# Performance work log

Measured on AMD Instinct MI355X. Metric: run time of the kernel, lower is better.

## Reference

```python
import jax, jax.numpy as jnp
import numpy as np

BOX = 256
SIGMA = 1.5
KS = 9  # int(ceil(6*sigma)), made odd
N_POINTS = 20000
N_NEURONS = 32
N_LAYERS = 3
LATENT = 8
BATCH = 16


def _make_kernel2(ks, sigma):
    ax = np.arange(ks) - ks // 2
    yy, xx = np.meshgrid(ax, ax, indexing='ij')
    k = np.exp(-(xx ** 2 + yy ** 2) / (2.0 * sigma ** 2))
    return (k / k.sum()).astype(np.float32)


def setup_inputs() -> dict:
    key = jax.random.key(0)
    ks = jax.random.split(key, 16)
    def n(k, shape, scale=1.0):
        return scale * jax.random.normal(k, shape, dtype=jnp.float32)
    return {
        'z': n(ks[0], (BATCH, LATENT)),
        'r': n(ks[1], (BATCH, 3, 3)),
        'pos': 0.1 * (jax.random.uniform(ks[2], (N_POINTS, 3), dtype=jnp.float32) - 0.5),
        'amp': 0.1 * jnp.ones((1,), jnp.float32),
        'linamp1_W': n(ks[3], (N_NEURONS, 4), 0.3),
        'ampblock_W': n(ks[4], (N_LAYERS, N_NEURONS, N_NEURONS), 0.1),
        'ampblock_b': n(ks[5], (N_LAYERS, N_NEURONS), 0.05),
        'linamp2_W': n(ks[6], (1, N_NEURONS), 0.1),
        'linamp2_b': n(ks[7], (1,), 0.05),
        'lin0_W': n(ks[8], (N_NEURONS, 3 + LATENT - 1), 0.3),
        'deform_W': n(ks[9], (N_LAYERS, N_NEURONS, N_NEURONS), 0.1),
        'deform_b': n(ks[10], (N_LAYERS, N_NEURONS), 0.05),
        'lin1a_W': n(ks[11], (3, N_NEURONS), 0.2),
        'lin1b_W': n(ks[12], (3, 3), 0.2),
        'k2': jnp.asarray(_make_kernel2(KS, SIGMA)),
        'd': 1,
    }


def _res_mlp(x, Ws, bs):
    # residual blocks: x <- relu(x @ W^T + b) + x
    for i in range(Ws.shape[0]):
        x = jax.nn.relu(x @ Ws[i].T + bs[i]) + x
    return x


def _splat(proj, amps, k2):
    # Gaussian-kernel splat of points onto [B, BOX, BOX] images.
    # proj: [B,P,2] coords in ~[-0.5, 0.5]; amps: [B,P]; k2: [KS,KS]
    B, P, _ = proj.shape
    ks = k2.shape[0]
    half = ks // 2
    pix = (proj + 0.5) * (BOX - 1)
    cx = jnp.round(pix[..., 0]).astype(jnp.int32)
    cy = jnp.round(pix[..., 1]).astype(jnp.int32)
    offs = jnp.arange(ks, dtype=jnp.int32) - half
    oy, ox = jnp.meshgrid(offs, offs, indexing='ij')
    xx = cx[:, :, None] + ox.reshape(-1)[None, None, :]   # [B,P,ks*ks]
    yy = cy[:, :, None] + oy.reshape(-1)[None, None, :]
    w = amps[:, :, None] * k2.reshape(-1)[None, None, :]
    valid = (xx >= 0) & (xx < BOX) & (yy >= 0) & (yy < BOX)
    bidx = jnp.arange(B, dtype=jnp.int32)[:, None, None]
    flat = jnp.where(valid, (bidx * BOX + yy) * BOX + xx, 0)
    img = jnp.zeros((B * BOX * BOX,), proj.dtype).at[flat.reshape(-1)].add(
        jnp.where(valid, w, jnp.zeros_like(w)).reshape(-1))
    return img.reshape(B, BOX, BOX)


def _forward(z, r, pos, amp, linamp1_W, ampblock_W, ampblock_b, linamp2_W,
             linamp2_b, lin0_W, deform_W, deform_b, lin1a_W, lin1b_W, k2, d):
    B = z.shape[0]
    P = pos.shape[0]
    posi = jnp.broadcast_to(pos[None], (B, P, 3))
    # amplitude head (diff_conf=True): last latent channel per point
    conf_a = jnp.broadcast_to(z[:, -1:][:, None, :], (B, P, 1))
    a = jnp.concatenate([posi, conf_a], axis=-1) @ linamp1_W.T
    a = _res_mlp(a, ampblock_W, ampblock_b)
    amp_corr = jax.nn.sigmoid(a @ linamp2_W.T + linamp2_b)  # [B,P,1]
    # deformation head on remaining latent channels
    if d > 0:
        conf = jnp.broadcast_to(z[:, :-1][:, None, :], (B, P, z.shape[1] - 1))
        res = jnp.concatenate([posi, conf], axis=-1) @ lin0_W.T
        res = _res_mlp(res, deform_W, deform_b)
        res = jnp.tanh(res @ lin1a_W.T)
        res = res @ lin1b_W.T
        pos_def = posi + res
    else:
        res = jnp.zeros_like(posi)
        pos_def = posi
    # project rotated points to 2D
    proj_pos = jnp.einsum('bij,bpj->bpi', r, pos_def)[..., :2]
    amps = amp * amp_corr[..., 0]  # [B,P]
    proj_im = _splat(proj_pos, amps, k2)
    return proj_im, pos_def, res, amp_corr


def reference(z, r, pos, amp, linamp1_W, ampblock_W, ampblock_b, linamp2_W,
              linamp2_b, lin0_W, deform_W, deform_b, lin1a_W, lin1b_W, k2, d):
    return _forward(z, r, pos, amp, linamp1_W, ampblock_W, ampblock_b,
                    linamp2_W, linamp2_b, lin0_W, deform_W, deform_b,
                    lin1a_W, lin1b_W, k2, d)
```

## Files before the change

### kernel.cpp

```cpp
#include <hip/hip_runtime.h>

#define BOX   256
#define KS    9
#define HALF  4
#define NPTS  20000
#define NB    16
#define NN    32
#define NL    3
#define NLAT  8
#define CANW  (BOX + 2 * HALF)

typedef _Float16 half8   __attribute__((ext_vector_type(8)));
typedef float    floatx4 __attribute__((ext_vector_type(4)));

#define WH_ELEMS      8192
#define LINAMP2_OFF   16384
#define LIN1A_OFF     16512
#define G_OFF         16896
#define CANVAS_OFF    20480
#define CANVAS_F4     ((NB * CANW * CANW) / 4)

__device__ __forceinline__ int perm_inv(int k) {
    return ((k >> 2) & 1) * 16 + (k >> 3) * 4 + (k & 3);
}

__global__ __launch_bounds__(256) void prep_kernel(
    const float* __restrict__ linamp1_W, const float* __restrict__ ampblock_W,
    const float* __restrict__ lin0_W, const float* __restrict__ deform_W,
    const float* __restrict__ lin1a_W, const float* __restrict__ linamp2_W,
    const float* __restrict__ k2, char* __restrict__ ws)
{
    const int idx = blockIdx.x * 256 + threadIdx.x;

    if (idx < CANVAS_F4) {
        floatx4 zv = {0.f, 0.f, 0.f, 0.f};
        ((floatx4*)(ws + CANVAS_OFF))[idx] = zv;
    }

    if (idx < WH_ELEMS) {
        _Float16* wh = (_Float16*)ws;
        const int mat = idx >> 10, rem = idx & 1023;
        const int m = rem >> 5, k = rem & 31;
        float v = 0.0f;
        if (mat == 0)      { if (k < 4)  v = linamp1_W[m * 4 + k]; }
        else if (mat <= 3) { v = ampblock_W[(mat - 1) * 1024 + m * 32 + perm_inv(k)]; }
        else if (mat == 4) { if (k < 10) v = lin0_W[m * 10 + k]; }
        else               { v = deform_W[(mat - 5) * 1024 + m * 32 + perm_inv(k)]; }
        wh[idx] = (_Float16)v;
    } else if (idx < WH_ELEMS + 32) {
        const int k = idx - WH_ELEMS;
        ((float*)(ws + LINAMP2_OFF))[k] = linamp2_W[perm_inv(k)];
    } else if (idx < WH_ELEMS + 32 + 96) {
        const int t = idx - (WH_ELEMS + 32);
        const int i = t >> 5, k = t & 31;
        ((float*)(ws + LIN1A_OFF))[t] = lin1a_W[i * 32 + perm_inv(k)];
    } else if (idx < WH_ELEMS + 32 + 96 + 9) {
        const int i = idx - (WH_ELEMS + 32 + 96);
        float s = 0.0f;
        #pragma unroll
        for (int j = 0; j < KS; ++j) s += k2[i * KS + j];
        ((float*)(ws + G_OFF))[i] = s;
    }
}

__global__ __launch_bounds__(256) void point_kernel(
    const float* __restrict__ z, const float* __restrict__ r,
    const float* __restrict__ pos, const float* __restrict__ amp,
    const float* __restrict__ ampblock_b, const float* __restrict__ linamp2_b,
    const float* __restrict__ deform_b, const float* __restrict__ lin1b_W,
    const int* __restrict__ dflag, const char* __restrict__ ws,
    float* __restrict__ canvas, float* __restrict__ pos_def_out,
    float* __restrict__ res_out, float* __restrict__ amp_corr_out)
{
    const _Float16* wh       = (const _Float16*)ws;
    const float*    linamp2p = (const float*)(ws + LINAMP2_OFF);
    const float*    lin1ap   = (const float*)(ws + LIN1A_OFF);

    const int tid  = blockIdx.x * 256 + threadIdx.x;
    const int lane = threadIdx.x & 63;
    const int n    = lane & 15;
    const int quad = lane >> 4;
    const int w    = tid >> 6;
    const int base_bp = w * 16;
    const int b    = base_bp / NPTS;
    const int base_p = base_bp - b * NPTS;
    const int p    = base_p + n;
    const int bp   = base_bp + n;
    const int d    = *dflag;

    const float px = pos[3 * p + 0];
    const float py = pos[3 * p + 1];
    const float pz = pos[3 * p + 2];
    float zv[NLAT];
    #pragma unroll
    for (int i = 0; i < NLAT; ++i) zv[i] = z[b * NLAT + i];

    const floatx4 zero = {0.f, 0.f, 0.f, 0.f};
    const int aoff = quad * 8;

    float xB[8];
    {
        half8 bf;
        #pragma unroll
        for (int j = 0; j < 8; ++j) bf[j] = (_Float16)0.f;
        if (quad == 0) {
            bf[0] = (_Float16)px; bf[1] = (_Float16)py;
            bf[2] = (_Float16)pz; bf[3] = (_Float16)zv[NLAT - 1];
        }
        half8 a0 = *(const half8*)(wh + (n)      * 32 + aoff);
        half8 a1 = *(const half8*)(wh + (n + 16) * 32 + aoff);
        floatx4 c0 = __builtin_amdgcn_mfma_f32_16x16x32_f16(a0, bf, zero, 0, 0, 0);
        floatx4 c1 = __builtin_amdgcn_mfma_f32_16x16x32_f16(a1, bf, zero, 0, 0, 0);
        #pragma unroll
        for (int rr = 0; rr < 4; ++rr) { xB[rr] = c0[rr]; xB[4 + rr] = c1[rr]; }
    }
    #pragma unroll
    for (int l = 0; l < NL; ++l) {
        half8 hf;
        #pragma unroll
        for (int j = 0; j < 8; ++j) hf[j] = (_Float16)xB[j];
        const _Float16* M = wh + (1 + l) * 1024;
        half8 a0 = *(const half8*)(M + (n)      * 32 + aoff);
        half8 a1 = *(const half8*)(M + (n + 16) * 32 + aoff);
        floatx4 d0 = __builtin_amdgcn_mfma_f32_16x16x32_f16(a0, hf, zero, 0, 0, 0);
        floatx4 d1 = __builtin_amdgcn_mfma_f32_16x16x32_f16(a1, hf, zero, 0, 0, 0);
        floatx4 b0 = *(const floatx4*)(ampblock_b + l * 32 + quad * 4);
        floatx4 b1 = *(const floatx4*)(ampblock_b + l * 32 + 16 + quad * 4);
        #pragma unroll
        for (int rr = 0; rr < 4; ++rr) {
            xB[rr]     += fmaxf(d0[rr] + b0[rr], 0.f);
            xB[4 + rr] += fmaxf(d1[rr] + b1[rr], 0.f);
        }
    }
    float corr;
    {
        floatx4 wa = *(const floatx4*)(linamp2p + aoff);
        floatx4 wb = *(const floatx4*)(linamp2p + aoff + 4);
        float s = 0.f;
        #pragma unroll
        for (int rr = 0; rr < 4; ++rr) s += wa[rr] * xB[rr] + wb[rr] * xB[4 + rr];
        s += __shfl_xor(s, 16);
        s += __shfl_xor(s, 32);
        corr = 1.f / (1.f + __expf(-(s + linamp2_b[0])));
    }

    float r0 = 0.f, r1 = 0.f, r2 = 0.f;
    if (d > 0) {
        {
            half8 bf;
            #pragma unroll
            for (int j = 0; j < 8; ++j) bf[j] = (_Float16)0.f;
            if (quad == 0) {
                bf[0] = (_Float16)px;    bf[1] = (_Float16)py;
                bf[2] = (_Float16)pz;    bf[3] = (_Float16)zv[0];
                bf[4] = (_Float16)zv[1]; bf[5] = (_Float16)zv[2];
                bf[6] = (_Float16)zv[3]; bf[7] = (_Float16)zv[4];
            } else if (quad == 1) {
                bf[0] = (_Float16)zv[5]; bf[1] = (_Float16)zv[6];
            }
            const _Float16* M = wh + 4 * 1024;
            half8 a0 = *(const half8*)(M + (n)      * 32 + aoff);
            half8 a1 = *(const half8*)(M + (n + 16) * 32 + aoff);
            floatx4 c0 = __builtin_amdgcn_mfma_f32_16x16x32_f16(a0, bf, zero, 0, 0, 0);
            floatx4 c1 = __builtin_amdgcn_mfma_f32_16x16x32_f16(a1, bf, zero, 0, 0, 0);
            #pragma unroll
            for (int rr = 0; rr < 4; ++rr) { xB[rr] = c0[rr]; xB[4 + rr] = c1[rr]; }
        }
        #pragma unroll
        for (int l = 0; l < NL; ++l) {
            half8 hf;
            #pragma unroll
            for (int j = 0; j < 8; ++j) hf[j] = (_Float16)xB[j];
            const _Float16* M = wh + (5 + l) * 1024;
            half8 a0 = *(const half8*)(M + (n)      * 32 + aoff);
            half8 a1 = *(const half8*)(M + (n + 16) * 32 + aoff);
            floatx4 d0 = __builtin_amdgcn_mfma_f32_16x16x32_f16(a0, hf, zero, 0, 0, 0);
            floatx4 d1 = __builtin_amdgcn_mfma_f32_16x16x32_f16(a1, hf, zero, 0, 0, 0);
            floatx4 b0 = *(const floatx4*)(deform_b + l * 32 + quad * 4);
            floatx4 b1 = *(const floatx4*)(deform_b + l * 32 + 16 + quad * 4);
            #pragma unroll
            for (int rr = 0; rr < 4; ++rr) {
                xB[rr]     += fmaxf(d0[rr] + b0[rr], 0.f);
                xB[4 + rr] += fmaxf(d1[rr] + b1[rr], 0.f);
            }
        }
        float t3[3];
        #pragma unroll
        for (int i = 0; i < 3; ++i) {
            floatx4 wa = *(const floatx4*)(lin1ap + i * 32 + aoff);
            floatx4 wb = *(const floatx4*)(lin1ap + i * 32 + aoff + 4);
            float s = 0.f;
            #pragma unroll
            for (int rr = 0; rr < 4; ++rr) s += wa[rr] * xB[rr] + wb[rr] * xB[4 + rr];
            s += __shfl_xor(s, 16);
            s += __shfl_xor(s, 32);
            t3[i] = 1.f - 2.f / (__expf(2.f * s) + 1.f);
        }
        r0 = t3[0] * lin1b_W[0] + t3[1] * lin1b_W[1] + t3[2] * lin1b_W[2];
        r1 = t3[0] * lin1b_W[3] + t3[1] * lin1b_W[4] + t3[2] * lin1b_W[5];
        r2 = t3[0] * lin1b_W[6] + t3[1] * lin1b_W[7] + t3[2] * lin1b_W[8];
    }

    const float pdx = px + r0, pdy = py + r1, pdz = pz + r2;

    if (quad == 0) {
        pos_def_out[3 * bp + 0] = pdx;
        pos_def_out[3 * bp + 1] = pdy;
        pos_def_out[3 * bp + 2] = pdz;
    } else if (quad == 1) {
        res_out[3 * bp + 0] = r0;
        res_out[3 * bp + 1] = r1;
        res_out[3 * bp + 2] = r2;
    } else if (quad == 2) {
        amp_corr_out[bp] = corr;
    } else {
        const float* rb = r + b * 9;
        const float pjx = rb[0] * pdx + rb[1] * pdy + rb[2] * pdz;
        const float pjy = rb[3] * pdx + rb[4] * pdy + rb[5] * pdz;
        const int cx = (int)rintf((pjx + 0.5f) * (float)(BOX - 1));
        const int cy = (int)rintf((pjy + 0.5f) * (float)(BOX - 1));
        if (cx >= -HALF && cx <= BOX - 1 + HALF &&
            cy >= -HALF && cy <= BOX - 1 + HALF) {
            atomicAdd(canvas + ((size_t)b * CANW + (cy + HALF)) * CANW + (cx + HALF),
                      amp[0] * corr);
        }
    }
}

__global__ __launch_bounds__(256) void conv_kernel(
    const float* __restrict__ canvas, const float* __restrict__ gws,
    float* __restrict__ img)
{
    __shared__ float t_lds[24][256];
    const int x  = threadIdx.x;
    const int b  = blockIdx.x >> 4;
    const int y0 = (blockIdx.x & 15) * 16;

    float g[KS];
    #pragma unroll
    for (int i = 0; i < KS; ++i) g[i] = gws[i];

    const float* cb = canvas + (size_t)b * CANW * CANW;
    #pragma unroll 4
    for (int rr = 0; rr < 24; ++rr) {
        const float* row = cb + (size_t)(y0 + rr) * CANW;
        float s = 0.f;
        #pragma unroll
        for (int i = 0; i < KS; ++i) s = fmaf(g[i], row[x + (KS - 1) - i], s);
        t_lds[rr][x] = s;
    }
    __syncthreads();

    float* ib = img + ((size_t)b * BOX + y0) * BOX;
    #pragma unroll 4
    for (int yy = 0; yy < 16; ++yy) {
        float s = 0.f;
        #pragma unroll
        for (int i = 0; i < KS; ++i) s = fmaf(g[i], t_lds[yy + (KS - 1) - i][x], s);
        ib[yy * BOX + x] = s;
    }
}

extern "C" void kernel_launch(void* const* d_in, const int* in_sizes, int n_in,
                              void* d_out, int out_size, void* d_ws, size_t ws_size,
                              hipStream_t stream) {
    const float* z          = (const float*)d_in[0];
    const float* r          = (const float*)d_in[1];
    const float* pos        = (const float*)d_in[2];
    const float* amp        = (const float*)d_in[3];
    const float* linamp1_W  = (const float*)d_in[4];
    const float* ampblock_W = (const float*)d_in[5];
    const float* ampblock_b = (const float*)d_in[6];
    const float* linamp2_W  = (const float*)d_in[7];
    const float* linamp2_b  = (const float*)d_in[8];
    const float* lin0_W     = (const float*)d_in[9];
    const float* deform_W   = (const float*)d_in[10];
    const float* deform_b   = (const float*)d_in[11];
    const float* lin1a_W    = (const float*)d_in[12];
    const float* lin1b_W    = (const float*)d_in[13];
    const float* k2         = (const float*)d_in[14];
    const int*   dflag      = (const int*)d_in[15];

    float* out = (float*)d_out;
    float* img          = out;
    float* pos_def_out  = out + (size_t)NB * BOX * BOX;
    float* res_out      = pos_def_out + (size_t)NB * NPTS * 3;
    float* amp_corr_out = res_out + (size_t)NB * NPTS * 3;

    char*  ws     = (char*)d_ws;
    float* gws    = (float*)(ws + G_OFF);
    float* canvas = (float*)(ws + CANVAS_OFF);

    prep_kernel<<<(CANVAS_F4 + 255) / 256, 256, 0, stream>>>(
        linamp1_W, ampblock_W, lin0_W, deform_W, lin1a_W, linamp2_W, k2, ws);

    point_kernel<<<5000, 256, 0, stream>>>(
        z, r, pos, amp, ampblock_b, linamp2_b, deform_b, lin1b_W, dflag,
        ws, canvas, pos_def_out, res_out, amp_corr_out);

    conv_kernel<<<NB * 16, 256, 0, stream>>>(canvas, gws, img);
}
```

Before: 143.3 us.

## Fuse prep, point MLP and separable conv into one persistent mega-kernel

Replaces the three launches with one memset plus a single kernel. Each block stages the fp16 weight matrices and biases in LDS and runs four 16-point groups per wave so weight fragments are reused. The last 128 blocks to finish, found through an atomic ticket counter, spin until all blocks are done and then run the separable Gaussian conv from LDS-staged canvas rows. This removes the launch gaps and the global weight reads, but it adds spin-waiting, a larger per-block LDS footprint and more register pressure.

Result: slower. 201.6 us (+40.7%).

```diff
diff --git a/kernel.cpp b/kernel.cpp
--- a/kernel.cpp
+++ b/kernel.cpp
@@ -5,259 +5,296 @@
 #define HALF  4
 #define NPTS  20000
 #define NB    16
-#define NN    32
-#define NL    3
 #define NLAT  8
-#define CANW  (BOX + 2 * HALF)
+#define CANW  264
+#define NBLK  1250
+#define NCONV 128
+#define CANVAS_ELEMS (NB * CANW * CANW)
 
 typedef _Float16 half8   __attribute__((ext_vector_type(8)));
 typedef float    floatx4 __attribute__((ext_vector_type(4)));
 
-#define WH_ELEMS      8192
-#define LINAMP2_OFF   16384
-#define LIN1A_OFF     16512
-#define G_OFF         16896
-#define CANVAS_OFF    20480
-#define CANVAS_F4     ((NB * CANW * CANW) / 4)
+#define CANVAS_BYTE_OFF 16
+
+#define SM_BYTES 49920
 
 __device__ __forceinline__ int perm_inv(int k) {
     return ((k >> 2) & 1) * 16 + (k >> 3) * 4 + (k & 3);
 }
 
-__global__ __launch_bounds__(256) void prep_kernel(
+__global__ __launch_bounds__(256, 2) void mega_kernel(
+    const float* __restrict__ z, const float* __restrict__ r,
+    const float* __restrict__ pos, const float* __restrict__ amp,
     const float* __restrict__ linamp1_W, const float* __restrict__ ampblock_W,
-    const float* __restrict__ lin0_W, const float* __restrict__ deform_W,
-    const float* __restrict__ lin1a_W, const float* __restrict__ linamp2_W,
-    const float* __restrict__ k2, char* __restrict__ ws)
+    const float* __restrict__ ampblock_b, const float* __restrict__ linamp2_W,
+    const float* __restrict__ linamp2_b, const float* __restrict__ lin0_W,
+    const float* __restrict__ deform_W, const float* __restrict__ deform_b,
+    const float* __restrict__ lin1a_W, const float* __restrict__ lin1b_W,
+    const float* __restrict__ k2, const int* __restrict__ dflag,
+    int* __restrict__ counter, float* __restrict__ canvas,
+    float* __restrict__ img, float* __restrict__ pos_def_out,
+    float* __restrict__ res_out, float* __restrict__ amp_corr_out)
 {
-    const int idx = blockIdx.x * 256 + threadIdx.x;
-
-    if (idx < CANVAS_F4) {
-        floatx4 zv = {0.f, 0.f, 0.f, 0.f};
-        ((floatx4*)(ws + CANVAS_OFF))[idx] = zv;
-    }
-
-    if (idx < WH_ELEMS) {
-        _Float16* wh = (_Float16*)ws;
-        const int mat = idx >> 10, rem = idx & 1023;
-        const int m = rem >> 5, k = rem & 31;
-        float v = 0.0f;
+    __shared__ __align__(16) char smem[SM_BYTES];
+    __shared__ int s_tk;
+    _Float16* wh       = (_Float16*)smem;
+    float*    linamp2p = (float*)(smem + 16384);
+    float*    lin1ap   = (float*)(smem + 16512);
+    float*    ampb     = (float*)(smem + 16896);
+    float*    defb     = (float*)(smem + 17280);
+
+    for (int e = threadIdx.x; e < 8192; e += 256) {
+        const int mat = e >> 10, rem = e & 1023, m = rem >> 5, k = rem & 31;
+        float v = 0.f;
         if (mat == 0)      { if (k < 4)  v = linamp1_W[m * 4 + k]; }
         else if (mat <= 3) { v = ampblock_W[(mat - 1) * 1024 + m * 32 + perm_inv(k)]; }
         else if (mat == 4) { if (k < 10) v = lin0_W[m * 10 + k]; }
         else               { v = deform_W[(mat - 5) * 1024 + m * 32 + perm_inv(k)]; }
-        wh[idx] = (_Float16)v;
-    } else if (idx < WH_ELEMS + 32) {
-        const int k = idx - WH_ELEMS;
-        ((float*)(ws + LINAMP2_OFF))[k] = linamp2_W[perm_inv(k)];
-    } else if (idx < WH_ELEMS + 32 + 96) {
-        const int t = idx - (WH_ELEMS + 32);
-        const int i = t >> 5, k = t & 31;
-        ((float*)(ws + LIN1A_OFF))[t] = lin1a_W[i * 32 + perm_inv(k)];
-    } else if (idx < WH_ELEMS + 32 + 96 + 9) {
-        const int i = idx - (WH_ELEMS + 32 + 96);
-        float s = 0.0f;
-        #pragma unroll
-        for (int j = 0; j < KS; ++j) s += k2[i * KS + j];
-        ((float*)(ws + G_OFF))[i] = s;
-    }
-}
-
-__global__ __launch_bounds__(256) void point_kernel(
-    const float* __restrict__ z, const float* __restrict__ r,
-    const float* __restrict__ pos, const float* __restrict__ amp,
-    const float* __restrict__ ampblock_b, const float* __restrict__ linamp2_b,
-    const float* __restrict__ deform_b, const float* __restrict__ lin1b_W,
-    const int* __restrict__ dflag, const char* __restrict__ ws,
-    float* __restrict__ canvas, float* __restrict__ pos_def_out,
-    float* __restrict__ res_out, float* __restrict__ amp_corr_out)
-{
-    const _Float16* wh       = (const _Float16*)ws;
-    const float*    linamp2p = (const float*)(ws + LINAMP2_OFF);
-    const float*    lin1ap   = (const float*)(ws + LIN1A_OFF);
-
-    const int tid  = blockIdx.x * 256 + threadIdx.x;
+        wh[e] = (_Float16)v;
+    }
+    if (threadIdx.x < 32) linamp2p[threadIdx.x] = linamp2_W[perm_inv(threadIdx.x)];
+    if (threadIdx.x < 96) {
+        lin1ap[threadIdx.x] = lin1a_W[(threadIdx.x >> 5) * 32 + perm_inv(threadIdx.x & 31)];
+        ampb[threadIdx.x]   = ampblock_b[threadIdx.x];
+        defb[threadIdx.x]   = deform_b[threadIdx.x];
+    }
+    __syncthreads();
+
     const int lane = threadIdx.x & 63;
     const int n    = lane & 15;
     const int quad = lane >> 4;
-    const int w    = tid >> 6;
-    const int base_bp = w * 16;
-    const int b    = base_bp / NPTS;
-    const int base_p = base_bp - b * NPTS;
-    const int p    = base_p + n;
-    const int bp   = base_bp + n;
+    const int aoff = quad * 8;
+    const int s    = blockIdx.x * 4 + (threadIdx.x >> 6);
     const int d    = *dflag;
-
-    const float px = pos[3 * p + 0];
-    const float py = pos[3 * p + 1];
-    const float pz = pos[3 * p + 2];
-    float zv[NLAT];
+    const float ampv = amp[0];
+    const float l2b  = linamp2_b[0];
+    const floatx4 zero = {0.f, 0.f, 0.f, 0.f};
+
+    {
+        int   bb[4];
+        float px[4], py[4], pz[4];
+        half8 bfa[4], bfd[4];
+        #pragma unroll
+        for (int g = 0; g < 4; ++g) {
+            const int base_bp = s * 64 + g * 16;
+            const int b = base_bp / NPTS;
+            const int p = base_bp - b * NPTS + n;
+            bb[g] = b;
+            px[g] = pos[3 * p + 0];
+            py[g] = pos[3 * p + 1];
+            pz[g] = pos[3 * p + 2];
+            float zl[NLAT];
+            #pragma unroll
+            for (int k = 0; k < NLAT; ++k) zl[k] = z[b * NLAT + k];
+            half8 t;
+            #pragma unroll
+            for (int j = 0; j < 8; ++j) t[j] = (_Float16)0.f;
+            bfa[g] = t; bfd[g] = t;
+            if (quad == 0) {
+                bfa[g][0] = (_Float16)px[g]; bfa[g][1] = (_Float16)py[g];
+                bfa[g][2] = (_Float16)pz[g]; bfa[g][3] = (_Float16)zl[7];
+                bfd[g][0] = (_Float16)px[g]; bfd[g][1] = (_Float16)py[g];
+                bfd[g][2] = (_Float16)pz[g]; bfd[g][3] = (_Float16)zl[0];
+                bfd[g][4] = (_Float16)zl[1]; bfd[g][5] = (_Float16)zl[2];
+                bfd[g][6] = (_Float16)zl[3]; bfd[g][7] = (_Float16)zl[4];
+            } else if (quad == 1) {
+                bfd[g][0] = (_Float16)zl[5]; bfd[g][1] = (_Float16)zl[6];
+            }
+        }
+
+        float xB[4][8];
+        {
+            half8 a0 = *(const half8*)(wh + n * 32 + aoff);
+            half8 a1 = *(const half8*)(wh + (n + 16) * 32 + aoff);
+            #pragma unroll
+            for (int g = 0; g < 4; ++g) {
+                floatx4 c0 = __builtin_amdgcn_mfma_f32_16x16x32_f16(a0, bfa[g], zero, 0, 0, 0);
+                floatx4 c1 = __builtin_amdgcn_mfma_f32_16x16x32_f16(a1, bfa[g], zero, 0, 0, 0);
+                #pragma unroll
+                for (int rr = 0; rr < 4; ++rr) { xB[g][rr] = c0[rr]; xB[g][4 + rr] = c1[rr]; }
+            }
+        }
+        #pragma unroll
+        for (int l = 0; l < 3; ++l) {
+            const _Float16* M = wh + (1 + l) * 1024;
+            half8 a0 = *(const half8*)(M + n * 32 + aoff);
+            half8 a1 = *(const half8*)(M + (n + 16) * 32 + aoff);
+            floatx4 b0 = *(const floatx4*)(ampb + l * 32 + quad * 4);
+            floatx4 b1 = *(const floatx4*)(ampb + l * 32 + 16 + quad * 4);
+            #pragma unroll
+            for (int g = 0; g < 4; ++g) {
+                half8 hf;
+                #pragma unroll
+                for (int j = 0; j < 8; ++j) hf[j] = (_Float16)xB[g][j];
+                floatx4 d0 = __builtin_amdgcn_mfma_f32_16x16x32_f16(a0, hf, zero, 0, 0, 0);
+                floatx4 d1 = __builtin_amdgcn_mfma_f32_16x16x32_f16(a1, hf, zero, 0, 0, 0);
+                #pragma unroll
+                for (int rr = 0; rr < 4; ++rr) {
+                    xB[g][rr]     += fmaxf(d0[rr] + b0[rr], 0.f);
+                    xB[g][4 + rr] += fmaxf(d1[rr] + b1[rr], 0.f);
+                }
+            }
+        }
+        float corr[4];
+        {
+            floatx4 wa = *(const floatx4*)(linamp2p + aoff);
+            floatx4 wb = *(const floatx4*)(linamp2p + aoff + 4);
+            #pragma unroll
+            for (int g = 0; g < 4; ++g) {
+                float sd = 0.f;
+                #pragma unroll
+                for (int rr = 0; rr < 4; ++rr) sd += wa[rr] * xB[g][rr] + wb[rr] * xB[g][4 + rr];
+                sd += __shfl_xor(sd, 16);
+                sd += __shfl_xor(sd, 32);
+                corr[g] = 1.f / (1.f + __expf(-(sd + l2b)));
+            }
+        }
+
+        float r0[4] = {0.f,0.f,0.f,0.f}, r1[4] = {0.f,0.f,0.f,0.f}, r2[4] = {0.f,0.f,0.f,0.f};
+        if (d > 0) {
+            {
+                const _Float16* M = wh + 4 * 1024;
+                half8 a0 = *(const half8*)(M + n * 32 + aoff);
+                half8 a1 = *(const half8*)(M + (n + 16) * 32 + aoff);
+                #pragma unroll
+                for (int g = 0; g < 4; ++g) {
+                    floatx4 c0 = __builtin_amdgcn_mfma_f32_16x16x32_f16(a0, bfd[g], zero, 0, 0, 0);
+                    floatx4 c1 = __builtin_amdgcn_mfma_f32_16x16x32_f16(a1, bfd[g], zero, 0, 0, 0);
+                    #pragma unroll
+                    for (int rr = 0; rr < 4; ++rr) { xB[g][rr] = c0[rr]; xB[g][4 + rr] = c1[rr]; }
+                }
+            }
+            #pragma unroll
+            for (int l = 0; l < 3; ++l) {
+                const _Float16* M = wh + (5 + l) * 1024;
+                half8 a0 = *(const half8*)(M + n * 32 + aoff);
+                half8 a1 = *(const half8*)(M + (n + 16) * 32 + aoff);
+                floatx4 b0 = *(const floatx4*)(defb + l * 32 + quad * 4);
+                floatx4 b1 = *(const floatx4*)(defb + l * 32 + 16 + quad * 4);
+                #pragma unroll
+                for (int g = 0; g < 4; ++g) {
+                    half8 hf;
+                    #pragma unroll
+                    for (int j = 0; j < 8; ++j) hf[j] = (_Float16)xB[g][j];
+                    floatx4 d0 = __builtin_amdgcn_mfma_f32_16x16x32_f16(a0, hf, zero, 0, 0, 0);
+                    floatx4 d1 = __builtin_amdgcn_mfma_f32_16x16x32_f16(a1, hf, zero, 0, 0, 0);
+                    #pragma unroll
+                    for (int rr = 0; rr < 4; ++rr) {
+                        xB[g][rr]     += fmaxf(d0[rr] + b0[rr], 0.f);
+                        xB[g][4 + rr] += fmaxf(d1[rr] + b1[rr], 0.f);
+                    }
+                }
+            }
+            #pragma unroll
+            for (int g = 0; g < 4; ++g) {
+                float t3[3];
+                #pragma unroll
+                for (int i = 0; i < 3; ++i) {
+                    floatx4 wa = *(const floatx4*)(lin1ap + i * 32 + aoff);
+                    floatx4 wb = *(const floatx4*)(lin1ap + i * 32 + aoff + 4);
+                    float sd = 0.f;
+                    #pragma unroll
+                    for (int rr = 0; rr < 4; ++rr) sd += wa[rr] * xB[g][rr] + wb[rr] * xB[g][4 + rr];
+                    sd += __shfl_xor(sd, 16);
+                    sd += __shfl_xor(sd, 32);
+                    t3[i] = 1.f - 2.f / (__expf(2.f * sd) + 1.f);
+                }
+                r0[g] = t3[0] * lin1b_W[0] + t3[1] * lin1b_W[1] + t3[2] * lin1b_W[2];
+                r1[g] = t3[0] * lin1b_W[3] + t3[1] * lin1b_W[4] + t3[2] * lin1b_W[5];
+                r2[g] = t3[0] * lin1b_W[6] + t3[1] * lin1b_W[7] + t3[2] * lin1b_W[8];
+            }
+        }
+
+        #pragma unroll
+        for (int g = 0; g < 4; ++g) {
+            const int bp = s * 64 + g * 16 + n;
+            const float pdx = px[g] + r0[g], pdy = py[g] + r1[g], pdz = pz[g] + r2[g];
+            if (quad == 0) {
+                pos_def_out[3 * bp + 0] = pdx;
+                pos_def_out[3 * bp + 1] = pdy;
+                pos_def_out[3 * bp + 2] = pdz;
+            } else if (quad == 1) {
+                res_out[3 * bp + 0] = r0[g];
+                res_out[3 * bp + 1] = r1[g];
+                res_out[3 * bp + 2] = r2[g];
+            } else if (quad == 2) {
+                amp_corr_out[bp] = corr[g];
+            } else {
+                const float* rb = r + bb[g] * 9;
+                const float pjx = rb[0] * pdx + rb[1] * pdy + rb[2] * pdz;
+                const float pjy = rb[3] * pdx + rb[4] * pdy + rb[5] * pdz;
+                const int cx = (int)rintf((pjx + 0.5f) * (float)(BOX - 1));
+                const int cy = (int)rintf((pjy + 0.5f) * (float)(BOX - 1));
+                if (cx >= -HALF && cx <= BOX - 1 + HALF &&
+                    cy >= -HALF && cy <= BOX - 1 + HALF) {
+                    atomicAdd(canvas + ((size_t)bb[g] * CANW + (cy + HALF)) * CANW + (cx + HALF),
+                              ampv * corr[g]);
+                }
+            }
+        }
+    }
+
+    __syncthreads();
+    if (threadIdx.x == 0) {
+        s_tk = __hip_atomic_fetch_add(counter, 1, __ATOMIC_ACQ_REL,
+                                      __HIP_MEMORY_SCOPE_AGENT);
+    }
+    __syncthreads();
+    const int tk = s_tk;
+    if (tk < NBLK - NCONV) return;
+
+    if (threadIdx.x == 0) {
+        while (__hip_atomic_load(counter, __ATOMIC_ACQUIRE,
+                                 __HIP_MEMORY_SCOPE_AGENT) < NBLK) {
+            __builtin_amdgcn_s_sleep(2);
+        }
+    }
+    __syncthreads();
+
+    float g9[KS];
     #pragma unroll
-    for (int i = 0; i < NLAT; ++i) zv[i] = z[b * NLAT + i];
-
-    const floatx4 zero = {0.f, 0.f, 0.f, 0.f};
-    const int aoff = quad * 8;
-
-    float xB[8];
-    {
-        half8 bf;
+    for (int i = 0; i < KS; ++i) {
+        float sg = 0.f;
         #pragma unroll
-        for (int j = 0; j < 8; ++j) bf[j] = (_Float16)0.f;
-        if (quad == 0) {
-            bf[0] = (_Float16)px; bf[1] = (_Float16)py;
-            bf[2] = (_Float16)pz; bf[3] = (_Float16)zv[NLAT - 1];
-        }
-        half8 a0 = *(const half8*)(wh + (n)      * 32 + aoff);
-        half8 a1 = *(const half8*)(wh + (n + 16) * 32 + aoff);
-        floatx4 c0 = __builtin_amdgcn_mfma_f32_16x16x32_f16(a0, bf, zero, 0, 0, 0);
-        floatx4 c1 = __builtin_amdgcn_mfma_f32_16x16x32_f16(a1, bf, zero, 0, 0, 0);
-        #pragma unroll
-        for (int rr = 0; rr < 4; ++rr) { xB[rr] = c0[rr]; xB[4 + rr] = c1[rr]; }
-    }
-    #pragma unroll
-    for (int l = 0; l < NL; ++l) {
-        half8 hf;
-        #pragma unroll
-        for (int j = 0; j < 8; ++j) hf[j] = (_Float16)xB[j];
-        const _Float16* M = wh + (1 + l) * 1024;
-        half8 a0 = *(const half8*)(M + (n)      * 32 + aoff);
-        half8 a1 = *(const half8*)(M + (n + 16) * 32 + aoff);
-        floatx4 d0 = __builtin_amdgcn_mfma_f32_16x16x32_f16(a0, hf, zero, 0, 0, 0);
-        floatx4 d1 = __builtin_amdgcn_mfma_f32_16x16x32_f16(a1, hf, zero, 0, 0, 0);
-        floatx4 b0 = *(const floatx4*)(ampblock_b + l * 32 + quad * 4);
-        floatx4 b1 = *(const floatx4*)(ampblock_b + l * 32 + 16 + quad * 4);
-        #pragma unroll
-        for (int rr = 0; rr < 4; ++rr) {
-            xB[rr]     += fmaxf(d0[rr] + b0[rr], 0.f);
-            xB[4 + rr] += fmaxf(d1[rr] + b1[rr], 0.f);
-        }
-    }
-    float corr;
-    {
-        floatx4 wa = *(const floatx4*)(linamp2p + aoff);
-        floatx4 wb = *(const floatx4*)(linamp2p + aoff + 4);
-        float s = 0.f;
-        #pragma unroll
-        for (int rr = 0; rr < 4; ++rr) s += wa[rr] * xB[rr] + wb[rr] * xB[4 + rr];
-        s += __shfl_xor(s, 16);
-        s += __shfl_xor(s, 32);
-        corr = 1.f / (1.f + __expf(-(s + linamp2_b[0])));
-    }
-
-    float r0 = 0.f, r1 = 0.f, r2 = 0.f;
-    if (d > 0) {
-        {
-            half8 bf;
-            #pragma unroll
-            for (int j = 0; j < 8; ++j) bf[j] = (_Float16)0.f;
-            if (quad == 0) {
-                bf[0] = (_Float16)px;    bf[1] = (_Float16)py;
-                bf[2] = (_Float16)pz;    bf[3] = (_Float16)zv[0];
-                bf[4] = (_Float16)zv[1]; bf[5] = (_Float16)zv[2];
-                bf[6] = (_Float16)zv[3]; bf[7] = (_Float16)zv[4];
-            } else if (quad == 1) {
-                bf[0] = (_Float16)zv[5]; bf[1] = (_Float16)zv[6];
-            }
-            const _Float16* M = wh + 4 * 1024;
-            half8 a0 = *(const half8*)(M + (n)      * 32 + aoff);
-            half8 a1 = *(const half8*)(M + (n + 16) * 32 + aoff);
-            floatx4 c0 = __builtin_amdgcn_mfma_f32_16x16x32_f16(a0, bf, zero, 0, 0, 0);
-            floatx4 c1 = __builtin_amdgcn_mfma_f32_16x16x32_f16(a1, bf, zero, 0, 0, 0);
-            #pragma unroll
-            for (int rr = 0; rr < 4; ++rr) { xB[rr] = c0[rr]; xB[4 + rr] = c1[rr]; }
-        }
-        #pragma unroll
-        for (int l = 0; l < NL; ++l) {
-            half8 hf;
-            #pragma unroll
-            for (int j = 0; j < 8; ++j) hf[j] = (_Float16)xB[j];
-            const _Float16* M = wh + (5 + l) * 1024;
-            half8 a0 = *(const half8*)(M + (n)      * 32 + aoff);
-            half8 a1 = *(const half8*)(M + (n + 16) * 32 + aoff);
-            floatx4 d0 = __builtin_amdgcn_mfma_f32_16x16x32_f16(a0, hf, zero, 0, 0, 0);
-            floatx4 d1 = __builtin_amdgcn_mfma_f32_16x16x32_f16(a1, hf, zero, 0, 0, 0);
-            floatx4 b0 = *(const floatx4*)(deform_b + l * 32 + quad * 4);
-            floatx4 b1 = *(const floatx4*)(deform_b + l * 32 + 16 + quad * 4);
-            #pragma unroll
-            for (int rr = 0; rr < 4; ++rr) {
-                xB[rr]     += fmaxf(d0[rr] + b0[rr], 0.f);
-                xB[4 + rr] += fmaxf(d1[rr] + b1[rr], 0.f);
-            }
-        }
-        float t3[3];
-        #pragma unroll
-        for (int i = 0; i < 3; ++i) {
-            floatx4 wa = *(const floatx4*)(lin1ap + i * 32 + aoff);
-            floatx4 wb = *(const floatx4*)(lin1ap + i * 32 + aoff + 4);
-            float s = 0.f;
-            #pragma unroll
-            for (int rr = 0; rr < 4; ++rr) s += wa[rr] * xB[rr] + wb[rr] * xB[4 + rr];
-            s += __shfl_xor(s, 16);
-            s += __shfl_xor(s, 32);
-            t3[i] = 1.f - 2.f / (__expf(2.f * s) + 1.f);
-        }
-        r0 = t3[0] * lin1b_W[0] + t3[1] * lin1b_W[1] + t3[2] * lin1b_W[2];
-        r1 = t3[0] * lin1b_W[3] + t3[1] * lin1b_W[4] + t3[2] * lin1b_W[5];
-        r2 = t3[0] * lin1b_W[6] + t3[1] * lin1b_W[7] + t3[2] * lin1b_W[8];
-    }
-
-    const float pdx = px + r0, pdy = py + r1, pdz = pz + r2;
-
-    if (quad == 0) {
-        pos_def_out[3 * bp + 0] = pdx;
-        pos_def_out[3 * bp + 1] = pdy;
-        pos_def_out[3 * bp + 2] = pdz;
-    } else if (quad == 1) {
-        res_out[3 * bp + 0] = r0;
-        res_out[3 * bp + 1] = r1;
-        res_out[3 * bp + 2] = r2;
-    } else if (quad == 2) {
-        amp_corr_out[bp] = corr;
-    } else {
-        const float* rb = r + b * 9;
-        const float pjx = rb[0] * pdx + rb[1] * pdy + rb[2] * pdz;
-        const float pjy = rb[3] * pdx + rb[4] * pdy + rb[5] * pdz;
-        const int cx = (int)rintf((pjx + 0.5f) * (float)(BOX - 1));
-        const int cy = (int)rintf((pjy + 0.5f) * (float)(BOX - 1));
-        if (cx >= -HALF && cx <= BOX - 1 + HALF &&
-            cy >= -HALF && cy <= BOX - 1 + HALF) {
-            atomicAdd(canvas + ((size_t)b * CANW + (cy + HALF)) * CANW + (cx + HALF),
-                      amp[0] * corr);
-        }
-    }
-}
-
-__global__ __launch_bounds__(256) void conv_kernel(
-    const float* __restrict__ canvas, const float* __restrict__ gws,
-    float* __restrict__ img)
-{
-    __shared__ float t_lds[24][256];
-    const int x  = threadIdx.x;
-    const int b  = blockIdx.x >> 4;
-    const int y0 = (blockIdx.x & 15) * 16;
-
-    float g[KS];
-    #pragma unroll
-    for (int i = 0; i < KS; ++i) g[i] = gws[i];
-
-    const float* cb = canvas + (size_t)b * CANW * CANW;
-    #pragma unroll 4
-    for (int rr = 0; rr < 24; ++rr) {
-        const float* row = cb + (size_t)(y0 + rr) * CANW;
-        float s = 0.f;
-        #pragma unroll
-        for (int i = 0; i < KS; ++i) s = fmaf(g[i], row[x + (KS - 1) - i], s);
-        t_lds[rr][x] = s;
-    }
-    __syncthreads();
-
-    float* ib = img + ((size_t)b * BOX + y0) * BOX;
-    #pragma unroll 4
-    for (int yy = 0; yy < 16; ++yy) {
-        float s = 0.f;
-        #pragma unroll
-        for (int i = 0; i < KS; ++i) s = fmaf(g[i], t_lds[yy + (KS - 1) - i][x], s);
-        ib[yy * BOX + x] = s;
+        for (int j = 0; j < KS; ++j) sg += k2[i * KS + j];
+        g9[i] = sg;
+    }
+
+    float* Cf = (float*)smem;
+    float* Tf = Cf + 24 * CANW;
+    const int x = threadIdx.x;
+
+    for (int sp = 0; sp < 2; ++sp) {
+        const int sidx = (tk - (NBLK - NCONV)) * 2 + sp;
+        const int b  = sidx >> 4;
+        const int y0 = (sidx & 15) * 16;
+        const float* cb = canvas + (size_t)b * CANW * CANW + (size_t)y0 * CANW;
+
+        for (int i = threadIdx.x; i < 24 * CANW; i += 256)
+            Cf[i] = __hip_atomic_load(cb + i, __ATOMIC_RELAXED,
+                                      __HIP_MEMORY_SCOPE_AGENT);
+        __syncthreads();
+
+        #pragma unroll 4
+        for (int rr = 0; rr < 24; ++rr) {
+            float sacc = 0.f;
+            #pragma unroll
+            for (int i = 0; i < KS; ++i)
+                sacc = fmaf(g9[i], Cf[rr * CANW + x + (KS - 1) - i], sacc);
+            Tf[rr * 256 + x] = sacc;
+        }
+        __syncthreads();
+
+        float* ib = img + ((size_t)b * BOX + y0) * BOX;
+        #pragma unroll 4
+        for (int yy = 0; yy < 16; ++yy) {
+            float sacc = 0.f;
+            #pragma unroll
+            for (int i = 0; i < KS; ++i)
+                sacc = fmaf(g9[i], Tf[(yy + (KS - 1) - i) * 256 + x], sacc);
+            ib[yy * BOX + x] = sacc;
+        }
+        __syncthreads();
     }
 }
 
@@ -287,16 +324,15 @@
     float* res_out      = pos_def_out + (size_t)NB * NPTS * 3;
     float* amp_corr_out = res_out + (size_t)NB * NPTS * 3;
 
-    char*  ws     = (char*)d_ws;
-    float* gws    = (float*)(ws + G_OFF);
-    float* canvas = (float*)(ws + CANVAS_OFF);
-
-    prep_kernel<<<(CANVAS_F4 + 255) / 256, 256, 0, stream>>>(
-        linamp1_W, ampblock_W, lin0_W, deform_W, lin1a_W, linamp2_W, k2, ws);
-
-    point_kernel<<<5000, 256, 0, stream>>>(
-        z, r, pos, amp, ampblock_b, linamp2_b, deform_b, lin1b_W, dflag,
-        ws, canvas, pos_def_out, res_out, amp_corr_out);
-
-    conv_kernel<<<NB * 16, 256, 0, stream>>>(canvas, gws, img);
+    int*   counter = (int*)d_ws;
+    float* canvas  = (float*)((char*)d_ws + CANVAS_BYTE_OFF);
+
+    hipMemsetAsync(d_ws, 0,
+                   CANVAS_BYTE_OFF + (size_t)CANVAS_ELEMS * sizeof(float),
+                   stream);
+
+    mega_kernel<<<NBLK, 256, 0, stream>>>(
+        z, r, pos, amp, linamp1_W, ampblock_W, ampblock_b, linamp2_W,
+        linamp2_b, lin0_W, deform_W, deform_b, lin1a_W, lin1b_W, k2, dflag,
+        counter, canvas, img, pos_def_out, res_out, amp_corr_out);
 }
```
